# Performance work log

Hardware: AMD Instinct MI355X
Metric: run time of the kernel (lower is better)

The kernel has to match this reference:

```python
import jax, jax.numpy as jnp
import numpy as np

DT = 0.001  # integration time step (forward arg dt in the original module)


def force_fn(x):
    # Harmonic well stand-in for the user-supplied force function.
    return -x


def _nh_step(x, v, alpha, kT, mass, Q):
    """One Nose-Hoover step, exactly mirroring the recompute block in backward()."""
    ndof = x.shape[-1]
    v2 = (v * v).sum(-1)
    alpha = alpha + (DT / 4) * (v2 - ndof * kT) / Q
    v = v * jnp.exp(-alpha[..., None] * (DT / 2))
    v2 = (v * v).sum(-1)
    alpha = alpha + (DT / 4) * (v2 - ndof * kT) / Q
    v = v + (DT / 2) * force_fn(x) / mass
    x = x + DT * v
    v = v + (DT / 2) * force_fn(x) / mass
    v2 = (v * v).sum(-1)
    alpha = alpha + (DT / 4) * (v2 - ndof * kT) / Q
    v = v * jnp.exp(-alpha[..., None] * (DT / 2))
    v2 = (v * v).sum(-1)
    alpha = alpha + (DT / 4) * (v2 - ndof * kT) / Q
    return x, v, alpha


def setup_inputs() -> dict:
    key = jax.random.key(0)
    k1, k2 = jax.random.split(key)
    B, D = 4096, 64  # batch of systems, degrees of freedom per system
    return {
        "x0": jax.random.normal(k1, (B, D), jnp.float32),
        "v0": jax.random.normal(k2, (B, D), jnp.float32),
        "alpha0": jnp.zeros((B,), jnp.float32),
        "kT": jnp.ones((), jnp.float32),
        "mass": jnp.ones((), jnp.float32),
        "Q": jnp.ones((), jnp.float32),
        "n_steps": 1000,
        "store_every": 10,
    }


def reference(x0, v0, alpha0, kT, mass, Q, n_steps, store_every):
    n_chunks = n_steps // store_every  # assume divisibility (1000 / 10)

    def inner(c, _):
        x, v, a = c
        return _nh_step(x, v, a, kT, mass, Q), None

    def chunk(c, _):
        c, _ = jax.lax.scan(inner, c, None, length=store_every)
        return c, (c[0], c[1])  # snapshot (x, v) every store_every steps

    _, (xs, vs) = jax.lax.scan(chunk, (x0, v0, alpha0), None, length=n_chunks)
    traj_x = jnp.concatenate([x0[None], xs], axis=0)  # [n_steps//store_every + 1, B, D]
    traj_v = jnp.concatenate([v0[None], vs], axis=0)
    return traj_x, traj_v
```

## Files before the change

kernel.cpp:

```cpp
#include <hip/hip_runtime.h>

#define DT 0.001f

typedef float f2 __attribute__((ext_vector_type(2)));

__device__ __forceinline__ float red32(float t) {
    t += __shfl_xor(t, 1,  64);
    t += __shfl_xor(t, 2,  64);
    t += __shfl_xor(t, 4,  64);
    t += __shfl_xor(t, 8,  64);
    t += __shfl_xor(t, 16, 64);
    return t;
}

template<int SE>
__global__ __launch_bounds__(256) void nh_fused(
    const float* __restrict__ x0, const float* __restrict__ v0,
    const float* __restrict__ alpha0,
    const float* __restrict__ kT_p, const float* __restrict__ mass_p,
    const float* __restrict__ Q_p,
    const int* __restrict__ n_steps_p, const int* __restrict__ store_every_p,
    float* __restrict__ out, int B)
{
    const int gid = blockIdx.x * 256 + threadIdx.x;
    const int sys = gid >> 5;
    const int g   = gid & 31;
    if (sys >= B) return;

    const int n_steps = *n_steps_p;
    const int se_rt   = *store_every_p;
    const int se      = (SE > 0) ? SE : se_rt;
    const int n_chunks = n_steps / se_rt;

    const int D = 64;
    const float kt = *kT_p, m = *mass_p, q = *Q_p;
    const float c   = 0.25f * DT / q;
    const float E   = (float)D * kt;
    const float cE  = c * E;
    const float c2  = 2.0f * c;
    const float c2E = 2.0f * cE;
    const float M2C2E = -2.0f * c2E;
    const float hd  = 0.5f * DT / m;
    const float hdt = 0.5f * DT;

    const float A11 = 1.0f - hd * DT;
    const float A21 = -hd * (2.0f - hd * DT);
    const float Ph1 = -hdt, Ph2 = 0.5f * hdt * hdt;
    const float Pf1 = -DT,  Pf2 = 0.5f * DT * DT;
    const float kc1 = -c2 * DT;
    const float kc2 = 0.5f * c2 * DT * DT;
    const float G00 = 1.0f - Ph1 * c2E;
    const float G01 = Ph1 * c2;
    const float G10 = 2.0f * Ph1;
    const float G11 = Ph1 * kc1;
    const float G2P = 4.0f * Ph2;

    const int snapF2 = B * 32;
    const int fidx   = sys * 32 + g;

    const f2 xv = ((const f2*)x0)[fidx];
    const f2 vv = ((const f2*)v0)[fidx];

    f2* outx = (f2*)out;
    f2* outv = outx + (size_t)(n_chunks + 1) * snapF2;

    __builtin_nontemporal_store(xv, &outx[fidx]);
    __builtin_nontemporal_store(vv, &outv[fidx]);

    float Sxx = red32(xv.x * xv.x + xv.y * xv.y);
    float Svv = red32(vv.x * vv.x + vv.y * vv.y);
    float Sxv = red32(xv.x * vv.x + xv.y * vv.y);
    float tSxv = 2.0f * Sxv;

    const float al0 = alpha0[sys];
    const float a1  = __builtin_fmaf(c, Svv, al0 - cE);
    float sv  = __builtin_fmaf(a1, __builtin_fmaf(a1, Ph2, Ph1), 1.0f);
    const float s1q0 = __builtin_fmaf(a1, __builtin_fmaf(a1, Pf2, Pf1), 1.0f);
    const float r1 = Svv * s1q0;
    float alm = __builtin_fmaf(c, r1, a1 - c2E);

    float pc00 = 1.f, pc01 = 0.f, pc10 = 0.f, pc11 = 1.f;

    for (int ck = 1; ck <= n_chunks; ++ck) {
        float m00 = 1.f, m01 = 0.f, m10 = 0.f, m11 = 1.f;
        float q0 = A11, q1 = 0.f, p0 = A21, p1 = 0.f;
        #pragma unroll
        for (int i = 0; i < se - 1; ++i) {
            const float b = sv * DT;
            const float d = sv * A11;
            const float n00 = __builtin_fmaf(b, m10, q0);
            const float n01 = __builtin_fmaf(b, m11, q1);
            const float n10 = __builtin_fmaf(d, m10, p0);
            const float n11 = __builtin_fmaf(d, m11, p1);
            const float u1 = __builtin_fmaf(tSxv, n11, Sxx * n10);
            const float r  = __builtin_fmaf(Svv, n11 * n11, n10 * u1);
            const float a3 = __builtin_fmaf(c, r, alm);
            const float g0 = __builtin_fmaf(G01, r, G00);
            const float g1 = __builtin_fmaf(G11, r, G10);
            const float svn = __builtin_fmaf(a3, __builtin_fmaf(a3, G2P, g1), g0);
            const float k0m = __builtin_fmaf(c2, r, M2C2E);
            const float k1  = __builtin_fmaf(kc1, r, 1.0f);
            const float k2  = kc2 * r;
            const float a4m = __builtin_fmaf(a3, __builtin_fmaf(a3, k2, k1), k0m);
            alm = __builtin_fmaf(c * r, svn * svn, a4m);
            m00 = n00; m01 = n01; m10 = n10; m11 = n11;
            q0 = A11 * n00; q1 = A11 * n01;
            p0 = A21 * n00; p1 = A21 * n01;
            sv = svn;
        }
        const float b = sv * DT;
        const float d = sv * A11;
        const float n00 = __builtin_fmaf(b, m10, q0);
        const float n01 = __builtin_fmaf(b, m11, q1);
        const float n10 = __builtin_fmaf(d, m10, p0);
        const float n11 = __builtin_fmaf(d, m11, p1);
        const float u1 = __builtin_fmaf(tSxv, n11, Sxx * n10);
        const float r  = __builtin_fmaf(Svv, n11 * n11, n10 * u1);
        const float a3 = __builtin_fmaf(c, r, alm);
        const float s2  = __builtin_fmaf(a3, __builtin_fmaf(a3, Ph2, Ph1), 1.0f);
        const float s2q = __builtin_fmaf(a3, __builtin_fmaf(a3, Pf2, Pf1), 1.0f);
        const float w2 = s2 * n10;
        const float w3 = s2 * n11;
        const float t00 = __builtin_fmaf(n00, pc00, n01 * pc10);
        const float t01 = __builtin_fmaf(n00, pc01, n01 * pc11);
        const float t10 = __builtin_fmaf(w2,  pc00, w3  * pc10);
        const float t11 = __builtin_fmaf(w2,  pc01, w3  * pc11);
        pc00 = t00; pc01 = t01; pc10 = t10; pc11 = t11;
        const f2 xe = pc00 * xv + pc01 * vv;
        const f2 ve = pc10 * xv + pc11 * vv;
        __builtin_nontemporal_store(xe, &outx[(size_t)ck * snapF2 + fidx]);
        __builtin_nontemporal_store(ve, &outv[(size_t)ck * snapF2 + fidx]);
        const float SxxN = __builtin_fmaf(n00 * n00, Sxx,
                             __builtin_fmaf(n00 * n01, tSxv, n01 * n01 * Svv));
        const float SxvN = __builtin_fmaf(w2 * n00, Sxx,
                             __builtin_fmaf(0.5f * __builtin_fmaf(n00, w3, n01 * w2), tSxv,
                                            n01 * w3 * Svv));
        const float SvvN = r * s2q;
        const float aU4 = __builtin_fmaf(c, SvvN, a3 - cE);
        const float aU1 = __builtin_fmaf(c, SvvN, aU4 - cE);
        const float s1n  = __builtin_fmaf(aU1, __builtin_fmaf(aU1, Ph2, Ph1), 1.0f);
        const float s1qn = __builtin_fmaf(aU1, __builtin_fmaf(aU1, Pf2, Pf1), 1.0f);
        alm = __builtin_fmaf(c * SvvN, s1qn, aU1 - c2E);
        sv = s1n;
        Sxx = SxxN; tSxv = 2.0f * SxvN; Svv = SvvN;
    }
}

extern "C" void kernel_launch(void* const* d_in, const int* in_sizes, int n_in,
                              void* d_out, int out_size, void* d_ws, size_t ws_size,
                              hipStream_t stream) {
    const float* x0     = (const float*)d_in[0];
    const float* v0     = (const float*)d_in[1];
    const float* alpha0 = (const float*)d_in[2];
    const float* kT     = (const float*)d_in[3];
    const float* mass   = (const float*)d_in[4];
    const float* Q      = (const float*)d_in[5];
    const int* n_steps  = (const int*)d_in[6];
    const int* store_ev = (const int*)d_in[7];

    const int B = in_sizes[0] / 64;
    const int threads = B * 32;
    const int block = 256;
    const int grid = (threads + block - 1) / block;

    nh_fused<10><<<grid, block, 0, stream>>>(
        x0, v0, alpha0, kT, mass, Q, n_steps, store_ev, (float*)d_out, B);
}
```

Before: 288.3 us.

## Parallelize time steps across wavefront lanes via fixed-point prefix-scan iteration

Replaces the per-system sequential step recurrence with a time-parallel scheme. Each 64-lane wavefront handles one system and processes blocks of 50 steps, one step per lane. Three fixed-point passes of shuffle-based prefix products of 2x2 step matrices and prefix sums of thermostat increments approximate the sequential thermostat trajectory. Snapshots are taken by broadcasting the cumulative matrix from the right lane. This trades the long serial dependency chain for many shuffles and twice as many threads. Accuracy depends on three passes converging for the nonlinear alpha update, and the per-lane sums use 64 lanes instead of 32 pairs.

```diff
diff --git a/kernel.cpp b/kernel.cpp
--- a/kernel.cpp
+++ b/kernel.cpp
@@ -2,19 +2,13 @@
 
 #define DT 0.001f
 
-typedef float f2 __attribute__((ext_vector_type(2)));
-
-__device__ __forceinline__ float red32(float t) {
-    t += __shfl_xor(t, 1,  64);
-    t += __shfl_xor(t, 2,  64);
-    t += __shfl_xor(t, 4,  64);
-    t += __shfl_xor(t, 8,  64);
-    t += __shfl_xor(t, 16, 64);
+__device__ __forceinline__ float red64(float t) {
+    t += __shfl_xor(t, 1);  t += __shfl_xor(t, 2);  t += __shfl_xor(t, 4);
+    t += __shfl_xor(t, 8);  t += __shfl_xor(t, 16); t += __shfl_xor(t, 32);
     return t;
 }
 
-template<int SE>
-__global__ __launch_bounds__(256) void nh_fused(
+__global__ __launch_bounds__(256) void nh_tp(
     const float* __restrict__ x0, const float* __restrict__ v0,
     const float* __restrict__ alpha0,
     const float* __restrict__ kT_p, const float* __restrict__ mass_p,
@@ -22,15 +16,14 @@
     const int* __restrict__ n_steps_p, const int* __restrict__ store_every_p,
     float* __restrict__ out, int B)
 {
-    const int gid = blockIdx.x * 256 + threadIdx.x;
-    const int sys = gid >> 5;
-    const int g   = gid & 31;
+    const int lane = threadIdx.x & 63;
+    const int sys  = blockIdx.x * 4 + (threadIdx.x >> 6);
     if (sys >= B) return;
 
     const int n_steps = *n_steps_p;
-    const int se_rt   = *store_every_p;
-    const int se      = (SE > 0) ? SE : se_rt;
-    const int n_chunks = n_steps / se_rt;
+    const int se      = *store_every_p;
+    const int n_chunks = n_steps / se;
+    const int n_blocks = n_steps / 50;
 
     const int D = 64;
     const float kt = *kT_p, m = *mass_p, q = *Q_p;
@@ -55,94 +48,111 @@
     const float G11 = Ph1 * kc1;
     const float G2P = 4.0f * Ph2;
 
-    const int snapF2 = B * 32;
-    const int fidx   = sys * 32 + g;
+    const int   base  = sys * 64 + lane;
+    const size_t snapN = (size_t)B * 64;
 
-    const f2 xv = ((const f2*)x0)[fidx];
-    const f2 vv = ((const f2*)v0)[fidx];
+    const float xe = x0[base];
+    const float ue = v0[base];
 
-    f2* outx = (f2*)out;
-    f2* outv = outx + (size_t)(n_chunks + 1) * snapF2;
+    float* outx = out;
+    float* outv = out + (size_t)(n_chunks + 1) * snapN;
 
-    __builtin_nontemporal_store(xv, &outx[fidx]);
-    __builtin_nontemporal_store(vv, &outv[fidx]);
+    __builtin_nontemporal_store(xe, &outx[base]);
+    __builtin_nontemporal_store(ue, &outv[base]);
 
-    float Sxx = red32(xv.x * xv.x + xv.y * xv.y);
-    float Svv = red32(vv.x * vv.x + vv.y * vv.y);
-    float Sxv = red32(xv.x * vv.x + xv.y * vv.y);
-    float tSxv = 2.0f * Sxv;
+    float Sxx  = red64(xe * xe);
+    float Svv  = red64(ue * ue);
+    float tSxv = 2.0f * red64(xe * ue);
 
     const float al0 = alpha0[sys];
     const float a1  = __builtin_fmaf(c, Svv, al0 - cE);
-    float sv  = __builtin_fmaf(a1, __builtin_fmaf(a1, Ph2, Ph1), 1.0f);
+    float sig_in = __builtin_fmaf(a1, __builtin_fmaf(a1, Ph2, Ph1), 1.0f);
     const float s1q0 = __builtin_fmaf(a1, __builtin_fmaf(a1, Pf2, Pf1), 1.0f);
-    const float r1 = Svv * s1q0;
-    float alm = __builtin_fmaf(c, r1, a1 - c2E);
+    float alm_in = __builtin_fmaf(c, Svv * s1q0, a1 - c2E);
 
-    float pc00 = 1.f, pc01 = 0.f, pc10 = 0.f, pc11 = 1.f;
+    float P00 = 1.f, P01 = 0.f, P10 = 0.f, P11 = 1.f;
 
-    for (int ck = 1; ck <= n_chunks; ++ck) {
-        float m00 = 1.f, m01 = 0.f, m10 = 0.f, m11 = 1.f;
-        float q0 = A11, q1 = 0.f, p0 = A21, p1 = 0.f;
+    for (int b = 0; b < n_blocks; ++b) {
+        float sig = sig_in;
+        float alm = alm_in;
+        float m00, m01, m10, m11, r, g0, g1, svn, a3;
+
         #pragma unroll
-        for (int i = 0; i < se - 1; ++i) {
-            const float b = sv * DT;
-            const float d = sv * A11;
-            const float n00 = __builtin_fmaf(b, m10, q0);
-            const float n01 = __builtin_fmaf(b, m11, q1);
-            const float n10 = __builtin_fmaf(d, m10, p0);
-            const float n11 = __builtin_fmaf(d, m11, p1);
-            const float u1 = __builtin_fmaf(tSxv, n11, Sxx * n10);
-            const float r  = __builtin_fmaf(Svv, n11 * n11, n10 * u1);
-            const float a3 = __builtin_fmaf(c, r, alm);
-            const float g0 = __builtin_fmaf(G01, r, G00);
-            const float g1 = __builtin_fmaf(G11, r, G10);
-            const float svn = __builtin_fmaf(a3, __builtin_fmaf(a3, G2P, g1), g0);
+        for (int pass = 0; pass < 3; ++pass) {
+            m00 = A11; m01 = sig * DT; m10 = A21; m11 = sig * A11;
+            #pragma unroll
+            for (int off = 1; off < 64; off <<= 1) {
+                float f00 = __shfl_up(m00, off), f01 = __shfl_up(m01, off);
+                float f10 = __shfl_up(m10, off), f11 = __shfl_up(m11, off);
+                if (lane < off) { f00 = 1.f; f01 = 0.f; f10 = 0.f; f11 = 1.f; }
+                const float n00 = __builtin_fmaf(m00, f00, m01 * f10);
+                const float n01 = __builtin_fmaf(m00, f01, m01 * f11);
+                const float n10 = __builtin_fmaf(m10, f00, m11 * f10);
+                const float n11 = __builtin_fmaf(m10, f01, m11 * f11);
+                m00 = n00; m01 = n01; m10 = n10; m11 = n11;
+            }
+            r = __builtin_fmaf(Svv, m11 * m11,
+                               m10 * __builtin_fmaf(tSxv, m11, Sxx * m10));
+            a3 = __builtin_fmaf(c, r, alm);
+            g0 = __builtin_fmaf(G01, r, G00);
+            g1 = __builtin_fmaf(G11, r, G10);
+            svn = __builtin_fmaf(a3, __builtin_fmaf(a3, G2P, g1), g0);
             const float k0m = __builtin_fmaf(c2, r, M2C2E);
             const float k1  = __builtin_fmaf(kc1, r, 1.0f);
             const float k2  = kc2 * r;
             const float a4m = __builtin_fmaf(a3, __builtin_fmaf(a3, k2, k1), k0m);
-            alm = __builtin_fmaf(c * r, svn * svn, a4m);
-            m00 = n00; m01 = n01; m10 = n10; m11 = n11;
-            q0 = A11 * n00; q1 = A11 * n01;
-            p0 = A21 * n00; p1 = A21 * n01;
-            sv = svn;
+            const float almn = __builtin_fmaf(c * r, svn * svn, a4m);
+            const float dlt = almn - alm;
+            float ps = dlt;
+            #pragma unroll
+            for (int off = 1; off < 64; off <<= 1) {
+                const float t = __shfl_up(ps, off);
+                ps += (lane >= off) ? t : 0.0f;
+            }
+            const float excl = __shfl_up(ps, 1);
+            alm = alm_in + ((lane == 0) ? 0.0f : excl);
+            a3 = __builtin_fmaf(c, r, alm);
+            svn = __builtin_fmaf(a3, __builtin_fmaf(a3, G2P, g1), g0);
+            const float t = __shfl_up(svn, 1);
+            sig = (lane == 0) ? sig_in : t;
         }
-        const float b = sv * DT;
-        const float d = sv * A11;
-        const float n00 = __builtin_fmaf(b, m10, q0);
-        const float n01 = __builtin_fmaf(b, m11, q1);
-        const float n10 = __builtin_fmaf(d, m10, p0);
-        const float n11 = __builtin_fmaf(d, m11, p1);
-        const float u1 = __builtin_fmaf(tSxv, n11, Sxx * n10);
-        const float r  = __builtin_fmaf(Svv, n11 * n11, n10 * u1);
-        const float a3 = __builtin_fmaf(c, r, alm);
-        const float s2  = __builtin_fmaf(a3, __builtin_fmaf(a3, Ph2, Ph1), 1.0f);
-        const float s2q = __builtin_fmaf(a3, __builtin_fmaf(a3, Pf2, Pf1), 1.0f);
-        const float w2 = s2 * n10;
-        const float w3 = s2 * n11;
-        const float t00 = __builtin_fmaf(n00, pc00, n01 * pc10);
-        const float t01 = __builtin_fmaf(n00, pc01, n01 * pc11);
-        const float t10 = __builtin_fmaf(w2,  pc00, w3  * pc10);
-        const float t11 = __builtin_fmaf(w2,  pc01, w3  * pc11);
-        pc00 = t00; pc01 = t01; pc10 = t10; pc11 = t11;
-        const f2 xe = pc00 * xv + pc01 * vv;
-        const f2 ve = pc10 * xv + pc11 * vv;
-        __builtin_nontemporal_store(xe, &outx[(size_t)ck * snapF2 + fidx]);
-        __builtin_nontemporal_store(ve, &outv[(size_t)ck * snapF2 + fidx]);
-        const float SxxN = __builtin_fmaf(n00 * n00, Sxx,
-                             __builtin_fmaf(n00 * n01, tSxv, n01 * n01 * Svv));
-        const float SxvN = __builtin_fmaf(w2 * n00, Sxx,
-                             __builtin_fmaf(0.5f * __builtin_fmaf(n00, w3, n01 * w2), tSxv,
-                                            n01 * w3 * Svv));
-        const float SvvN = r * s2q;
-        const float aU4 = __builtin_fmaf(c, SvvN, a3 - cE);
-        const float aU1 = __builtin_fmaf(c, SvvN, aU4 - cE);
-        const float s1n  = __builtin_fmaf(aU1, __builtin_fmaf(aU1, Ph2, Ph1), 1.0f);
-        const float s1qn = __builtin_fmaf(aU1, __builtin_fmaf(aU1, Pf2, Pf1), 1.0f);
-        alm = __builtin_fmaf(c * SvvN, s1qn, aU1 - c2E);
-        sv = s1n;
-        Sxx = SxxN; tSxv = 2.0f * SxvN; Svv = SvvN;
+
+        const float s2 = __builtin_fmaf(a3, __builtin_fmaf(a3, Ph2, Ph1), 1.0f);
+        const float q00 = __builtin_fmaf(m00, P00, m01 * P10);
+        const float q01 = __builtin_fmaf(m00, P01, m01 * P11);
+        const float q10 = s2 * __builtin_fmaf(m10, P00, m11 * P10);
+        const float q11 = s2 * __builtin_fmaf(m10, P01, m11 * P11);
+
+        const int bs = b * 50;
+        const int rm = bs % se;
+        for (int s = se - rm; s <= 50; s += se) {
+            const int l = s - 1;
+            const float b00 = __shfl(q00, l), b01 = __shfl(q01, l);
+            const float b10 = __shfl(q10, l), b11 = __shfl(q11, l);
+            const float sx = __builtin_fmaf(b00, xe, b01 * ue);
+            const float sv_ = __builtin_fmaf(b10, xe, b11 * ue);
+            const size_t ck = (size_t)(bs + s) / se;
+            __builtin_nontemporal_store(sx,  &outx[ck * snapN + base]);
+            __builtin_nontemporal_store(sv_, &outv[ck * snapN + base]);
+        }
+
+        const float M00 = __shfl(m00, 49), M01 = __shfl(m01, 49);
+        const float M10 = __shfl(m10, 49), M11 = __shfl(m11, 49);
+        const float nP00 = __builtin_fmaf(M00, P00, M01 * P10);
+        const float nP01 = __builtin_fmaf(M00, P01, M01 * P11);
+        const float nP10 = __builtin_fmaf(M10, P00, M11 * P10);
+        const float nP11 = __builtin_fmaf(M10, P01, M11 * P11);
+        P00 = nP00; P01 = nP01; P10 = nP10; P11 = nP11;
+        const float SxxN = __builtin_fmaf(M00 * M00, Sxx,
+                            __builtin_fmaf(M00 * M01, tSxv, M01 * M01 * Svv));
+        const float SvvN = __builtin_fmaf(M10 * M10, Sxx,
+                            __builtin_fmaf(M10 * M11, tSxv, M11 * M11 * Svv));
+        const float SxvN = __builtin_fmaf(M00 * M10, Sxx,
+                            __builtin_fmaf(0.5f * __builtin_fmaf(M00, M11, M01 * M10),
+                                           tSxv, M01 * M11 * Svv));
+        Sxx = SxxN; Svv = SvvN; tSxv = 2.0f * SxvN;
+        alm_in = __shfl(alm, 50);
+        sig_in = __shfl(sig, 50);
     }
 }
 
@@ -159,10 +169,10 @@
     const int* store_ev = (const int*)d_in[7];
 
     const int B = in_sizes[0] / 64;
-    const int threads = B * 32;
+    const int threads = B * 64;
     const int block = 256;
     const int grid = (threads + block - 1) / block;
 
-    nh_fused<10><<<grid, block, 0, stream>>>(
+    nh_tp<<<grid, block, 0, stream>>>(
         x0, v0, alpha0, kT, mass, Q, n_steps, store_ev, (float*)d_out, B);
 }
```

Result: slower. 302.7 us (+5.0%).
